# Kernel optimization log

Hardware: AMD Instinct MI355X
Metric: run time of the kernel (lower is better)

## Reference

```python
import jax, jax.numpy as jnp
import numpy as np

B, S, H = 2, 2048, 1024
E, I = 8, 4096
TOP_K = 2
W_SCALE = 0.02


def setup_inputs() -> dict:
    key = jax.random.key(0)
    k1, k2, k3, k4, k5 = jax.random.split(key, 5)
    return {
        "hidden_states": jax.random.normal(k1, (B, S, H), dtype=jnp.float32),
        "gate_w": jax.random.normal(k2, (H, E), dtype=jnp.float32) * W_SCALE,
        "w1s": jax.random.normal(k3, (E, H, I), dtype=jnp.float32) * W_SCALE,
        "w2s": jax.random.normal(k4, (E, I, H), dtype=jnp.float32) * W_SCALE,
        "w3s": jax.random.normal(k5, (E, H, I), dtype=jnp.float32) * W_SCALE,
    }


def reference(hidden_states, gate_w, w1s, w2s, w3s):
    b, s, h = hidden_states.shape
    x = hidden_states.reshape(-1, h)                      # [T, H]
    # Router: softmax in fp32, top-k, renormalize (matches torch F.softmax(dtype=float) + topk)
    logits = x @ gate_w                                   # [T, E]
    probs = jax.nn.softmax(logits.astype(jnp.float32), axis=-1)
    rw, sel = jax.lax.top_k(probs, TOP_K)                 # [T, K], [T, K]
    rw = rw / jnp.sum(rw, axis=-1, keepdims=True)
    # Per-token combine weight for each expert: [T, E]
    comb = jnp.sum(jax.nn.one_hot(sel, E, dtype=x.dtype) * rw[..., None].astype(x.dtype), axis=1)
    # Expert SwiGLU MLPs; loop over small fixed expert count (same math as grouped GEMM + scatter)
    out = jnp.zeros_like(x)
    for e in range(E):
        inter = jax.nn.silu(x @ w1s[e]) * (x @ w3s[e])    # [T, I]
        out = out + comb[:, e:e + 1] * (inter @ w2s[e])   # [T, H]
    return out.reshape(b, s, h)
```

## Files before the change

### kernel.cpp

```cpp
#include <hip/hip_runtime.h>

#define T_TOK 4096
#define H_DIM 1024
#define I_DIM 4096
#define NE 8
#define INTER_ROWS 9216

typedef _Float16 f16;
typedef _Float16 f16x8 __attribute__((ext_vector_type(8)));
typedef _Float16 f16x4 __attribute__((ext_vector_type(4)));
typedef float f32x4 __attribute__((ext_vector_type(4)));

#define GLOBAL_AS __attribute__((address_space(1)))
#define LDS_AS __attribute__((address_space(3)))

__device__ __forceinline__ void gload_lds16(const void* g, void* l) {
  __builtin_amdgcn_global_load_lds((GLOBAL_AS const unsigned int*)g,
                                   (LDS_AS unsigned int*)l, 16, 0, 0);
}

#define VM0() asm volatile("s_waitcnt vmcnt(0)" ::: "memory")
#define BARF()                          \
  do {                                  \
    asm volatile("" ::: "memory");      \
    __builtin_amdgcn_s_barrier();       \
    asm volatile("" ::: "memory");      \
  } while (0)
#define PRIO1() __builtin_amdgcn_s_setprio(1)
#define PRIO0() __builtin_amdgcn_s_setprio(0)

__global__ void cast_x_kernel(const float* __restrict__ x, f16* __restrict__ xh) {
  int i = blockIdx.x * 256 + threadIdx.x;
  float4 v = reinterpret_cast<const float4*>(x)[i];
  f16x4 o = {(f16)v.x, (f16)v.y, (f16)v.z, (f16)v.w};
  reinterpret_cast<f16x4*>(xh)[i] = o;
}

__global__ __launch_bounds__(256) void transpose_cast_kernel(
    const float* __restrict__ w1s, const float* __restrict__ w3s,
    const float* __restrict__ w2s, f16* __restrict__ w13t, f16* __restrict__ w2t) {
  __shared__ float tile[64][65];
  const int z = blockIdx.z;
  const int tr = threadIdx.x >> 4;
  const int tc = (threadIdx.x & 15) * 4;
  if (z < 16) {
    int e = z & 7;
    const float* in = (z < 8 ? w1s : w3s) + (size_t)e * H_DIM * I_DIM;
    f16* out = w13t + (size_t)e * (2 * H_DIM * I_DIM);
    const int roff = (z < 8) ? 0 : 32;
    const int c0 = blockIdx.x * 64, r0 = blockIdx.y * 64;
#pragma unroll
    for (int i = 0; i < 4; ++i) {
      int r = tr + i * 16;
      float4 v = *reinterpret_cast<const float4*>(&in[(size_t)(r0 + r) * I_DIM + c0 + tc]);
      tile[r][tc] = v.x; tile[r][tc + 1] = v.y; tile[r][tc + 2] = v.z; tile[r][tc + 3] = v.w;
    }
    __syncthreads();
#pragma unroll
    for (int it = 0; it < 2; ++it) {
      int idx = it * 256 + threadIdx.x;
      int oc = idx >> 3;
      int ch = (idx & 7) * 8;
      int cg = c0 + oc;
      int rowo = ((cg >> 5) << 6) + roff + (cg & 31);
      f16x8 h;
#pragma unroll
      for (int j = 0; j < 8; ++j) h[j] = (f16)tile[ch + j][oc];
      *reinterpret_cast<f16x8*>(&out[(size_t)rowo * H_DIM + r0 + ch]) = h;
    }
  } else {
    int e = z - 16;
    const float* in = w2s + (size_t)e * H_DIM * I_DIM;
    f16* out = w2t + (size_t)e * H_DIM * I_DIM;
    const int r0 = blockIdx.x * 64, c0 = blockIdx.y * 64;
#pragma unroll
    for (int i = 0; i < 4; ++i) {
      int r = tr + i * 16;
      float4 v = *reinterpret_cast<const float4*>(&in[(size_t)(r0 + r) * H_DIM + c0 + tc]);
      tile[r][tc] = v.x; tile[r][tc + 1] = v.y; tile[r][tc + 2] = v.z; tile[r][tc + 3] = v.w;
    }
    __syncthreads();
#pragma unroll
    for (int it = 0; it < 2; ++it) {
      int idx = it * 256 + threadIdx.x;
      int oc = idx >> 3;
      int ch = (idx & 7) * 8;
      f16x8 h;
#pragma unroll
      for (int j = 0; j < 8; ++j) h[j] = (f16)tile[ch + j][oc];
      *reinterpret_cast<f16x8*>(&out[(size_t)(c0 + oc) * I_DIM + r0 + ch]) = h;
    }
  }
}

__global__ void router_kernel(const float* __restrict__ x, const float* __restrict__ gw,
                              int* __restrict__ counts, int* __restrict__ lists,
                              float* __restrict__ wgts) {
  const int t = blockIdx.x;
  const int l = threadIdx.x;
  const float* xr = x + (size_t)t * H_DIM;
  float acc[NE];
#pragma unroll
  for (int e = 0; e < NE; ++e) acc[e] = 0.f;
  for (int k = l; k < H_DIM; k += 64) {
    float xv = xr[k];
#pragma unroll
    for (int e = 0; e < NE; ++e) acc[e] += xv * gw[k * NE + e];
  }
#pragma unroll
  for (int e = 0; e < NE; ++e) {
    float v = acc[e];
#pragma unroll
    for (int off = 32; off > 0; off >>= 1) v += __shfl_xor(v, off);
    acc[e] = v;
  }
  if (l == 0) {
    int i1 = 0;
#pragma unroll
    for (int e = 1; e < NE; ++e)
      if (acc[e] > acc[i1]) i1 = e;
    int i2 = (i1 == 0) ? 1 : 0;
#pragma unroll
    for (int e = 0; e < NE; ++e)
      if (e != i1 && acc[e] > acc[i2]) i2 = e;
    float wA = 1.f / (1.f + __expf(acc[i2] - acc[i1]));
    float wB = 1.f - wA;
    int p1 = atomicAdd(&counts[i1], 1);
    lists[i1 * T_TOK + p1] = t;
    wgts[i1 * T_TOK + p1] = wA;
    int p2 = atomicAdd(&counts[i2], 1);
    lists[i2 * T_TOK + p2] = t;
    wgts[i2 * T_TOK + p2] = wB;
  }
}

__global__ void prefix_kernel(const int* __restrict__ counts, int* __restrict__ bases) {
  if (threadIdx.x == 0) {
    int s = 0;
#pragma unroll
    for (int e = 0; e < NE; ++e) {
      bases[e] = s;
      s += (counts[e] + 127) & ~127;
    }
  }
}

#define LDAm(DST, kh, SBASE)                                                      \
  {                                                                               \
    _Pragma("unroll") for (int m_ = 0; m_ < 8; ++m_) {                            \
      int row = wm * 128 + m_ * 16 + lrow;                                        \
      DST[m_] = *reinterpret_cast<const f16x8*>(                                  \
          &SBASE[row * 64 + (((kh)*4 + lk) ^ (row & 7)) * 8]);                    \
    }                                                                             \
  }
#define LDBm(DST, kh, np, SBBASE)                                                 \
  {                                                                               \
    _Pragma("unroll") for (int n_ = 0; n_ < 2; ++n_) {                            \
      int row = wn * 64 + ((np)*2 + n_) * 16 + lrow;                              \
      DST[n_] = *reinterpret_cast<const f16x8*>(                                  \
          &SBBASE[row * 64 + (((kh)*4 + lk) ^ (row & 7)) * 8]);                   \
    }                                                                             \
  }
#define MFm(AF, BF, np)                                                           \
  {                                                                               \
    PRIO1();                                                                      \
    _Pragma("unroll") for (int m_ = 0; m_ < 8; ++m_)                              \
        _Pragma("unroll") for (int n_ = 0; n_ < 2; ++n_)                          \
            acc[m_][(np)*2 + n_] = __builtin_amdgcn_mfma_f32_16x16x32_f16(        \
                AF[m_], BF[n_], acc[m_][(np)*2 + n_], 0, 0, 0);                   \
    PRIO0();                                                                      \
  }

__global__ __launch_bounds__(512, 1) void gemm_a_kernel(
    const f16* __restrict__ xh, const f16* __restrict__ w13t,
    const int* __restrict__ counts, const int* __restrict__ bases,
    const int* __restrict__ lists, f16* __restrict__ inter) {
  const int w = blockIdx.x;
  const int xcd = w & 7, q = w >> 3;
  const int bx = xcd * 4 + (q & 3);
  const int by = q >> 2;
  const int z = blockIdx.z;
  const int cnt = counts[z];
  const int r0 = by * 256;
  if (r0 >= cnt) return;
  const int base = bases[z], pad = (cnt + 127) & ~127;
  const int c0 = bx * 256;
  const int tid = threadIdx.x, lane = tid & 63, wid = tid >> 6;
  const int wm = wid >> 2, wn = wid & 3, lrow = lane & 15, lk = lane >> 4;

  __shared__ __align__(16) f16 lds[2][32768];

  const int* lst = lists + z * T_TOK;
  const f16* w13 = w13t + (size_t)z * (2 * H_DIM * I_DIM);

  const f16* sp[4][2];
  f16* dp[4][2];
#pragma unroll
  for (int j = 0; j < 2; ++j) {
    int cg = (wid * 2 + j) * 64 + lane;
    int rih = cg >> 3;
    int loct = (cg & 7) ^ (rih & 7);
    int t0 = lst[r0 + rih], t1 = lst[r0 + 128 + rih];
    sp[0][j] = xh + (size_t)t0 * H_DIM + loct * 8;
    sp[2][j] = xh + (size_t)t1 * H_DIM + loct * 8;
    sp[1][j] = w13 + (size_t)(c0 + rih) * H_DIM + loct * 8;
    sp[3][j] = w13 + (size_t)(c0 + 128 + rih) * H_DIM + loct * 8;
    dp[0][j] = &lds[0][cg * 8];
    dp[2][j] = &lds[0][8192 + cg * 8];
    dp[1][j] = &lds[0][16384 + cg * 8];
    dp[3][j] = &lds[0][24576 + cg * 8];
  }

#define STG(u, S, K)                                        \
  do {                                                      \
    gload_lds16(sp[u][0] + (K), dp[u][0] + (S)*32768);      \
    gload_lds16(sp[u][1] + (K), dp[u][1] + (S)*32768);      \
  } while (0)

  const f32x4 z4 = {0.f, 0.f, 0.f, 0.f};
  f32x4 acc[8][4];
#pragma unroll
  for (int m = 0; m < 8; ++m)
#pragma unroll
    for (int n = 0; n < 4; ++n) acc[m][n] = z4;

  f16x8 afA[8], afB[8], bfX[2], bfY[2];
  const int NT = H_DIM / 64;

  STG(0, 0, 0); STG(1, 0, 0); STG(2, 0, 0); STG(3, 0, 0);
  VM0(); BARF();
  { const f16* SA = lds[0]; const f16* SB = SA + 16384;
    LDAm(afA, 0, SA); LDBm(bfX, 0, 0, SB); }

  for (int t = 0; t < NT; ++t) {
    const f16* SA = lds[t & 1];
    const f16* SB = SA + 16384;
    const int S = (t + 1) & 1;
    const f16* SA2 = lds[S];
    const f16* SB2 = SA2 + 16384;
    const bool more = (t + 1 < NT);
    const int ks = (t + 1) * 64;
    if (more) { STG(0, S, ks); STG(1, S, ks); }
    LDBm(bfY, 0, 1, SB);
    BARF();
    MFm(afA, bfX, 0);
    if (more) { STG(2, S, ks); STG(3, S, ks); }
    LDAm(afB, 1, SA);
    LDBm(bfX, 1, 0, SB);
    BARF();
    MFm(afA, bfY, 1);
    LDBm(bfY, 1, 1, SB);
    BARF();
    MFm(afB, bfX, 0);
    VM0();
    BARF();
    if (more) { LDAm(afA, 0, SA2); LDBm(bfX, 0, 0, SB2); }
    MFm(afB, bfY, 1);
  }
#undef STG

#pragma unroll
  for (int m = 0; m < 8; ++m)
#pragma unroll
    for (int r = 0; r < 4; ++r) {
      int rowl = wm * 128 + m * 16 + lk * 4 + r;
      if (r0 + rowl < pad) {
        size_t grow = base + r0 + rowl;
#pragma unroll
        for (int n = 0; n < 2; ++n) {
          int col = (c0 >> 1) + wn * 32 + n * 16 + lrow;
          float v1 = acc[m][n][r];
          float v3 = acc[m][n + 2][r];
          float sv = v1 / (1.f + __expf(-v1));
          inter[grow * I_DIM + col] = (f16)(sv * v3);
        }
      }
    }
}

__global__ __launch_bounds__(512, 1) void gemm_b_kernel(
    const f16* __restrict__ inter, const f16* __restrict__ w2t,
    const int* __restrict__ counts, const int* __restrict__ bases,
    const int* __restrict__ lists, const float* __restrict__ wgts,
    float* __restrict__ out) {
  const int w = blockIdx.x;
  const int xcd = w & 7, q = w >> 3;
  const int bx = xcd >> 1;
  const int yid = (xcd & 1) * 16 + q;
  const int rb = yid >> 1, kb = yid & 1;
  const int z = blockIdx.z;
  const int cnt = counts[z];
  const int r0 = rb * 256;
  if (r0 >= cnt) return;
  const int base = bases[z];
  const int c0 = bx * 256;
  const int tid = threadIdx.x, lane = tid & 63, wid = tid >> 6;
  const int wm = wid >> 2, wn = wid & 3, lrow = lane & 15, lk = lane >> 4;

  __shared__ __align__(16) f16 lds[2][32768];

  const int* lst = lists + z * T_TOK;
  const float* wgt = wgts + z * T_TOK;
  const f16* w2 = w2t + (size_t)z * I_DIM * H_DIM;
  const int K0 = kb * 2048;

  const f16* sp[4][2];
  f16* dp[4][2];
#pragma unroll
  for (int j = 0; j < 2; ++j) {
    int cg = (wid * 2 + j) * 64 + lane;
    int rih = cg >> 3;
    int loct = (cg & 7) ^ (rih & 7);
    sp[0][j] = inter + (size_t)(base + r0 + rih) * I_DIM + K0 + loct * 8;
    sp[2][j] = inter + (size_t)(base + r0 + 128 + rih) * I_DIM + K0 + loct * 8;
    sp[1][j] = w2 + (size_t)(c0 + rih) * I_DIM + K0 + loct * 8;
    sp[3][j] = w2 + (size_t)(c0 + 128 + rih) * I_DIM + K0 + loct * 8;
    dp[0][j] = &lds[0][cg * 8];
    dp[2][j] = &lds[0][8192 + cg * 8];
    dp[1][j] = &lds[0][16384 + cg * 8];
    dp[3][j] = &lds[0][24576 + cg * 8];
  }

#define STG(u, S, K)                                        \
  do {                                                      \
    gload_lds16(sp[u][0] + (K), dp[u][0] + (S)*32768);      \
    gload_lds16(sp[u][1] + (K), dp[u][1] + (S)*32768);      \
  } while (0)

  const f32x4 z4 = {0.f, 0.f, 0.f, 0.f};
  f32x4 acc[8][4];
#pragma unroll
  for (int m = 0; m < 8; ++m)
#pragma unroll
    for (int n = 0; n < 4; ++n) acc[m][n] = z4;

  f16x8 afA[8], afB[8], bfX[2], bfY[2];
  const int NT = 2048 / 64;

  STG(0, 0, 0); STG(1, 0, 0); STG(2, 0, 0); STG(3, 0, 0);
  VM0(); BARF();
  { const f16* SA = lds[0]; const f16* SB = SA + 16384;
    LDAm(afA, 0, SA); LDBm(bfX, 0, 0, SB); }

  for (int t = 0; t < NT; ++t) {
    const f16* SA = lds[t & 1];
    const f16* SB = SA + 16384;
    const int S = (t + 1) & 1;
    const f16* SA2 = lds[S];
    const f16* SB2 = SA2 + 16384;
    const bool more = (t + 1 < NT);
    const int ks = (t + 1) * 64;
    if (more) { STG(0, S, ks); STG(1, S, ks); }
    LDBm(bfY, 0, 1, SB);
    BARF();
    MFm(afA, bfX, 0);
    if (more) { STG(2, S, ks); STG(3, S, ks); }
    LDAm(afB, 1, SA);
    LDBm(bfX, 1, 0, SB);
    BARF();
    MFm(afA, bfY, 1);
    LDBm(bfY, 1, 1, SB);
    BARF();
    MFm(afB, bfX, 0);
    VM0();
    BARF();
    if (more) { LDAm(afA, 0, SA2); LDBm(bfX, 0, 0, SB2); }
    MFm(afB, bfY, 1);
  }
#undef STG

#pragma unroll
  for (int m = 0; m < 8; ++m)
#pragma unroll
    for (int r = 0; r < 4; ++r) {
      int ri = r0 + wm * 128 + m * 16 + lk * 4 + r;
      if (ri < cnt) {
        int tok = lst[ri];
        float wg = wgt[ri];
        float* orow = out + (size_t)tok * H_DIM + c0 + wn * 64 + lrow;
#pragma unroll
        for (int n = 0; n < 4; ++n) atomicAdd(&orow[n * 16], wg * acc[m][n][r]);
      }
    }
}

extern "C" void kernel_launch(void* const* d_in, const int* in_sizes, int n_in,
                              void* d_out, int out_size, void* d_ws, size_t ws_size,
                              hipStream_t stream) {
  const float* x = (const float*)d_in[0];
  const float* gw = (const float*)d_in[1];
  const float* w1s = (const float*)d_in[2];
  const float* w2s = (const float*)d_in[3];
  const float* w3s = (const float*)d_in[4];
  float* out = (float*)d_out;

  char* ws = (char*)d_ws;
  f16* xh = (f16*)ws;
  f16* inter = (f16*)(ws + ((size_t)8 << 20));
  f16* w13t = (f16*)(ws + ((size_t)80 << 20));
  f16* w2t = (f16*)(ws + ((size_t)208 << 20));
  char* meta = ws + ((size_t)272 << 20);
  int* counts = (int*)meta;
  int* bases = (int*)(meta + 512);
  int* lists = (int*)(meta + 1024);
  float* wgts = (float*)(meta + 1024 + (size_t)NE * T_TOK * 4);

  hipMemsetAsync(out, 0, (size_t)out_size * sizeof(float), stream);
  hipMemsetAsync(meta, 0, 1024 + (size_t)NE * T_TOK * 8, stream);

  cast_x_kernel<<<dim3((T_TOK * H_DIM) / (4 * 256)), dim3(256), 0, stream>>>(x, xh);
  router_kernel<<<dim3(T_TOK), dim3(64), 0, stream>>>(x, gw, counts, lists, wgts);
  prefix_kernel<<<dim3(1), dim3(64), 0, stream>>>(counts, bases);
  transpose_cast_kernel<<<dim3(64, 16, 24), dim3(256), 0, stream>>>(
      w1s, w3s, w2s, w13t, w2t);
  gemm_a_kernel<<<dim3(512, 1, NE), dim3(512), 0, stream>>>(
      xh, w13t, counts, bases, lists, inter);
  gemm_b_kernel<<<dim3(128, 1, NE), dim3(512), 0, stream>>>(
      inter, w2t, counts, bases, lists, wgts, out);
}
```

Measured before the change: 611.3 us.

## Drop XCD-aware block remap, split GEMM-B K four ways, narrow transpose stores

Removes the XCD-aware block-index swizzle in both GEMM kernels and uses plain 2D grid indexing. GEMM-B's split-K factor goes from 2 to 4, which doubles the number of blocks and halves each block's K loop. The cost is more atomic or accumulated partial writes into the output and possibly worse L2 locality across XCDs. The transpose-cast kernel now writes 4-wide fp16 stores instead of 8-wide ones.

Result: faster. 575.8 us (-5.8%).

```diff
diff --git a/kernel.cpp b/kernel.cpp
--- a/kernel.cpp
+++ b/kernel.cpp
@@ -57,16 +57,14 @@
     }
     __syncthreads();
 #pragma unroll
-    for (int it = 0; it < 2; ++it) {
-      int idx = it * 256 + threadIdx.x;
-      int oc = idx >> 3;
-      int ch = (idx & 7) * 8;
+    for (int i = 0; i < 4; ++i) {
+      int oc = tr + i * 16;
       int cg = c0 + oc;
       int rowo = ((cg >> 5) << 6) + roff + (cg & 31);
-      f16x8 h;
-#pragma unroll
-      for (int j = 0; j < 8; ++j) h[j] = (f16)tile[ch + j][oc];
-      *reinterpret_cast<f16x8*>(&out[(size_t)rowo * H_DIM + r0 + ch]) = h;
+      f16x4 h;
+#pragma unroll
+      for (int j = 0; j < 4; ++j) h[j] = (f16)tile[tc + j][oc];
+      *reinterpret_cast<f16x4*>(&out[(size_t)rowo * H_DIM + r0 + tc]) = h;
     }
   } else {
     int e = z - 16;
@@ -81,14 +79,12 @@
     }
     __syncthreads();
 #pragma unroll
-    for (int it = 0; it < 2; ++it) {
-      int idx = it * 256 + threadIdx.x;
-      int oc = idx >> 3;
-      int ch = (idx & 7) * 8;
-      f16x8 h;
-#pragma unroll
-      for (int j = 0; j < 8; ++j) h[j] = (f16)tile[ch + j][oc];
-      *reinterpret_cast<f16x8*>(&out[(size_t)(c0 + oc) * I_DIM + r0 + ch]) = h;
+    for (int i = 0; i < 4; ++i) {
+      int oc = tr + i * 16;
+      f16x4 h;
+#pragma unroll
+      for (int j = 0; j < 4; ++j) h[j] = (f16)tile[tc + j][oc];
+      *reinterpret_cast<f16x4*>(&out[(size_t)(c0 + oc) * I_DIM + r0 + tc]) = h;
     }
   }
 }
@@ -175,16 +171,12 @@
     const f16* __restrict__ xh, const f16* __restrict__ w13t,
     const int* __restrict__ counts, const int* __restrict__ bases,
     const int* __restrict__ lists, f16* __restrict__ inter) {
-  const int w = blockIdx.x;
-  const int xcd = w & 7, q = w >> 3;
-  const int bx = xcd * 4 + (q & 3);
-  const int by = q >> 2;
   const int z = blockIdx.z;
   const int cnt = counts[z];
-  const int r0 = by * 256;
+  const int r0 = blockIdx.y * 256;
   if (r0 >= cnt) return;
   const int base = bases[z], pad = (cnt + 127) & ~127;
-  const int c0 = bx * 256;
+  const int c0 = blockIdx.x * 256;
   const int tid = threadIdx.x, lane = tid & 63, wid = tid >> 6;
   const int wm = wid >> 2, wn = wid & 3, lrow = lane & 15, lk = lane >> 4;
 
@@ -283,17 +275,13 @@
     const int* __restrict__ counts, const int* __restrict__ bases,
     const int* __restrict__ lists, const float* __restrict__ wgts,
     float* __restrict__ out) {
-  const int w = blockIdx.x;
-  const int xcd = w & 7, q = w >> 3;
-  const int bx = xcd >> 1;
-  const int yid = (xcd & 1) * 16 + q;
-  const int rb = yid >> 1, kb = yid & 1;
   const int z = blockIdx.z;
   const int cnt = counts[z];
+  const int rb = blockIdx.y >> 2, kb = blockIdx.y & 3;
   const int r0 = rb * 256;
   if (r0 >= cnt) return;
   const int base = bases[z];
-  const int c0 = bx * 256;
+  const int c0 = blockIdx.x * 256;
   const int tid = threadIdx.x, lane = tid & 63, wid = tid >> 6;
   const int wm = wid >> 2, wn = wid & 3, lrow = lane & 15, lk = lane >> 4;
 
@@ -302,7 +290,7 @@
   const int* lst = lists + z * T_TOK;
   const float* wgt = wgts + z * T_TOK;
   const f16* w2 = w2t + (size_t)z * I_DIM * H_DIM;
-  const int K0 = kb * 2048;
+  const int K0 = kb * 1024;
 
   const f16* sp[4][2];
   f16* dp[4][2];
@@ -335,7 +323,7 @@
     for (int n = 0; n < 4; ++n) acc[m][n] = z4;
 
   f16x8 afA[8], afB[8], bfX[2], bfY[2];
-  const int NT = 2048 / 64;
+  const int NT = 1024 / 64;
 
   STG(0, 0, 0); STG(1, 0, 0); STG(2, 0, 0); STG(3, 0, 0);
   VM0(); BARF();
@@ -413,8 +401,8 @@
   prefix_kernel<<<dim3(1), dim3(64), 0, stream>>>(counts, bases);
   transpose_cast_kernel<<<dim3(64, 16, 24), dim3(256), 0, stream>>>(
       w1s, w3s, w2s, w13t, w2t);
-  gemm_a_kernel<<<dim3(512, 1, NE), dim3(512), 0, stream>>>(
+  gemm_a_kernel<<<dim3((2 * I_DIM) / 256, T_TOK / 256, NE), dim3(512), 0, stream>>>(
       xh, w13t, counts, bases, lists, inter);
-  gemm_b_kernel<<<dim3(128, 1, NE), dim3(512), 0, stream>>>(
+  gemm_b_kernel<<<dim3(H_DIM / 256, 4 * (T_TOK / 256), NE), dim3(512), 0, stream>>>(
       inter, w2t, counts, bases, lists, wgts, out);
 }
```
